# Kernel optimization log

Hardware: AMD Instinct MI355X
Metric: run time of the kernel (lower is better)

The kernel has to match this reference:

```python
import jax, jax.numpy as jnp
import numpy as np

TURBO_BLOCK_SIZE = 64
TURBO_MSE_BITS = 5
QMAX = 2 ** (TURBO_MSE_BITS - 1) - 1  # 15 for symmetric int5
# MSE scale search grid: shrink factors applied to the max-abs scale
SHRINKS = np.linspace(0.4, 1.0, 16)


def mse_quant_dequant(w):
    """Block-wise (block=64, along input dim) symmetric int5 quantize-dequantize.
    Per block, searches a grid of shrunken max-abs scales and keeps the one
    minimizing reconstruction MSE."""
    O, I = w.shape
    wb = w.reshape(O, I // TURBO_BLOCK_SIZE, TURBO_BLOCK_SIZE)
    amax = jnp.max(jnp.abs(wb), axis=-1, keepdims=True)
    base = jnp.maximum(amax, 1e-8) / QMAX
    best_err = jnp.full(amax.shape, jnp.inf, dtype=w.dtype)
    best_scale = base
    for s in SHRINKS:  # fixed small grid, not a data-dim loop
        scale = base * jnp.asarray(s, dtype=w.dtype)
        deq = jnp.clip(jnp.round(wb / scale), -QMAX, QMAX) * scale
        err = jnp.sum((deq - wb) ** 2, axis=-1, keepdims=True)
        upd = err < best_err
        best_err = jnp.where(upd, err, best_err)
        best_scale = jnp.where(upd, scale, best_scale)
    deq = jnp.clip(jnp.round(wb / best_scale), -QMAX, QMAX) * best_scale
    return deq.reshape(O, I)


def turbo_linear(x, w):
    # Straight-through estimator: forward uses quantized weights,
    # gradient flows to w as identity.
    wq = w + jax.lax.stop_gradient(mse_quant_dequant(w) - w)
    return x @ wq.T


def setup_inputs() -> dict:
    key = jax.random.key(0)
    k1, k2, k3 = jax.random.split(key, 3)
    dim, mlp_mult = 2048, 4
    hidden = mlp_mult * dim
    x = jax.random.normal(k1, (4, 2048, dim), dtype=jnp.float32)
    w_fc = jax.random.normal(k2, (hidden, dim), dtype=jnp.float32) * 0.02
    w_proj = jax.random.normal(k3, (dim, hidden), dtype=jnp.float32) * 0.02
    return {"x": x, "w_fc": w_fc, "w_proj": w_proj}


def reference(x, w_fc, w_proj):
    h = jnp.maximum(turbo_linear(x, w_fc), 0.0)  # relu
    return turbo_linear(h * h, w_proj)           # relu-square then proj
```

## Files before the change

### kernel.cpp

```cpp
#include <hip/hip_runtime.h>
#include <hip/hip_bf16.h>

typedef __attribute__((ext_vector_type(8))) __bf16 bf16x8;
typedef __attribute__((ext_vector_type(4))) float f32x4;

__device__ __forceinline__ void gload_lds16(const void* g, void* lds) {
    __builtin_amdgcn_global_load_lds(
        (const __attribute__((address_space(1))) void*)g,
        (__attribute__((address_space(3))) void*)lds, 16, 0, 0);
}

__global__ __launch_bounds__(256) void quant_bf16_kernel(
    const float* __restrict__ w, __hip_bfloat16* __restrict__ wq, int nblk)
{
#pragma clang fp contract(off)
    int b = blockIdx.x * 256 + threadIdx.x;
    if (b >= nblk) return;
    const float4* src = (const float4*)(w + (size_t)b * 64);
    float v[64];
#pragma unroll
    for (int i = 0; i < 16; ++i) {
        float4 t = src[i];
        v[i*4+0] = t.x; v[i*4+1] = t.y; v[i*4+2] = t.z; v[i*4+3] = t.w;
    }
    float amax = 0.0f;
#pragma unroll
    for (int i = 0; i < 64; ++i) amax = fmaxf(amax, fabsf(v[i]));
    float base = fmaxf(amax, 1e-8f) / 15.0f;

    float best_err = __builtin_inff();
    float best_scale = base, best_rs = 0.0f;
    for (int k = 0; k < 16; ++k) {
        double sd = (k == 15) ? 1.0 : ((double)k * (0.6 / 15.0) + 0.4);
        float scale = base * (float)sd;
        float rs = 1.0f / scale;
        float err = 0.0f;
#pragma unroll
        for (int i = 0; i < 64; ++i) {
            float q = rintf(v[i] * rs);
            q = fminf(fmaxf(q, -15.0f), 15.0f);
            float d = q * scale - v[i];
            err = err + d * d;
        }
        if (err < best_err) { best_err = err; best_scale = scale; best_rs = rs; }
    }
    __hip_bfloat16* dst = wq + (size_t)b * 64;
#pragma unroll
    for (int i = 0; i < 64; ++i) {
        float q = rintf(v[i] * best_rs);
        q = fminf(fmaxf(q, -15.0f), 15.0f);
        dst[i] = __float2bfloat16(q * best_scale);
    }
}

__global__ __launch_bounds__(256) void f32_to_bf16_kernel(
    const float* __restrict__ in, __hip_bfloat16* __restrict__ out, int n8)
{
    int i = blockIdx.x * 256 + threadIdx.x;
    if (i >= n8) return;
    const float4* p = (const float4*)(in + (size_t)i * 8);
    float4 a = p[0], b = p[1];
    alignas(16) __hip_bfloat16 r[8];
    r[0] = __float2bfloat16(a.x); r[1] = __float2bfloat16(a.y);
    r[2] = __float2bfloat16(a.z); r[3] = __float2bfloat16(a.w);
    r[4] = __float2bfloat16(b.x); r[5] = __float2bfloat16(b.y);
    r[6] = __float2bfloat16(b.z); r[7] = __float2bfloat16(b.w);
    *(uint4*)(out + (size_t)i * 8) = *(const uint4*)r;
}

#define SB0() __builtin_amdgcn_sched_barrier(0)
#define BARRIER() { SB0(); __builtin_amdgcn_s_barrier(); SB0(); }
#define STAGE(base, eoff, ldsOff) \
    gload_lds16((base) + (size_t)((eoff) + voff), smem + (ldsOff) + wOff)

template <int EPI>
__global__ __launch_bounds__(256, 2) void gemm256_kernel(
    const __hip_bfloat16* __restrict__ A,
    const __hip_bfloat16* __restrict__ B,
    void* __restrict__ Cout, int M, int N, int K)
{
    extern __shared__ char smem[];

    const int t    = threadIdx.x;
    const int lane = t & 63;
    const int w    = t >> 6;
    const int wr   = w >> 1;
    const int wc   = w & 1;
    const int lo   = lane & 15;
    const int hi   = lane >> 4;
    const uint wOff = (uint)w * 1024u;

    const int cpx = gridDim.x >> 3;
    int bid = blockIdx.x;
    bid = (bid & 7) * cpx + (bid >> 3);
    const int nN = N >> 7;
    const int bm = bid / nN;
    const int bn = bid % nN;
    const int rowBase = bm << 8;
    const int colBase = bn << 7;

    const __hip_bfloat16* uA = A + (size_t)rowBase * (size_t)K;
    const __hip_bfloat16* uB = B + (size_t)colBase * (size_t)K;

    const uint voff = ((uint)(t >> 2)) * (uint)K
                    + ((((uint)t & 3u) ^ (((uint)t >> 3) & 3u)) * 8u);
    const uint K64 = (uint)K * 64u;

    const uint laneOff = (uint)lo * 64u
                       + ((((uint)hi) ^ (((uint)lo >> 1) & 3u)) << 4);
    const uint aFB = (uint)wr * 8192u + laneOff;
    const uint bFB = 16384u + (uint)wc * 4096u + laneOff;

    f32x4 acc[8][4] = {};

    STAGE(uA, 0u,     0u);      STAGE(uA, K64,    4096u);
    STAGE(uA, 2u*K64, 8192u);   STAGE(uA, 3u*K64, 12288u);
    STAGE(uB, 0u,     16384u);  STAGE(uB, K64,    20480u);
    asm volatile("s_waitcnt vmcnt(0)" ::: "memory");
    BARRIER();

    const int NT = K >> 5;
    for (int tt = 0; tt < NT; ++tt) {
        const uint bufOff = (uint)(tt & 1) * 24576u;
        const uint nxtOff = bufOff ^ 24576u;
        const bool pf = (tt + 1 < NT);
        const uint kN = ((uint)(tt + 1)) << 5;

        if (pf) {
            STAGE(uA, kN,          nxtOff + 0u);
            STAGE(uA, kN + K64,    nxtOff + 4096u);
            STAGE(uA, kN + 2u*K64, nxtOff + 8192u);
            STAGE(uA, kN + 3u*K64, nxtOff + 12288u);
            STAGE(uB, kN,          nxtOff + 16384u);
            STAGE(uB, kN + K64,    nxtOff + 20480u);
        }
        SB0();

        bf16x8 bfr[4], afr[8];
#pragma unroll
        for (int j = 0; j < 4; ++j)
            bfr[j] = *(const bf16x8*)(smem + bufOff + bFB + (uint)j * 1024u);
#pragma unroll
        for (int i = 0; i < 8; ++i)
            afr[i] = *(const bf16x8*)(smem + bufOff + aFB + (uint)i * 1024u);

        __builtin_amdgcn_s_setprio(1);
#pragma unroll
        for (int i = 0; i < 8; ++i)
#pragma unroll
            for (int j = 0; j < 4; ++j)
                acc[i][j] = __builtin_amdgcn_mfma_f32_16x16x32_bf16(
                    afr[i], bfr[j], acc[i][j], 0, 0, 0);
        __builtin_amdgcn_s_setprio(0);

        if (pf) asm volatile("s_waitcnt vmcnt(0)" ::: "memory");
        BARRIER();
    }

    if (EPI == 0) {
        __hip_bfloat16* Cb = (__hip_bfloat16*)Cout;
#pragma unroll
        for (int i = 0; i < 8; ++i)
#pragma unroll
            for (int j = 0; j < 4; ++j)
#pragma unroll
                for (int r = 0; r < 4; ++r) {
                    size_t row = rowBase + wr*128 + i*16 + hi*4 + r;
                    size_t col = colBase + wc*64 + j*16 + lo;
                    float v = fmaxf(acc[i][j][r], 0.0f);
                    Cb[row * N + col] = __float2bfloat16(v * v);
                }
    } else {
        float* Cf = (float*)Cout;
#pragma unroll
        for (int i = 0; i < 8; ++i)
#pragma unroll
            for (int j = 0; j < 4; ++j)
#pragma unroll
                for (int r = 0; r < 4; ++r) {
                    size_t row = rowBase + wr*128 + i*16 + hi*4 + r;
                    size_t col = colBase + wc*64 + j*16 + lo;
                    Cf[row * N + col] = acc[i][j][r];
                }
    }
}

extern "C" void kernel_launch(void* const* d_in, const int* in_sizes, int n_in,
                              void* d_out, int out_size, void* d_ws, size_t ws_size,
                              hipStream_t stream) {
    const float* x      = (const float*)d_in[0];
    const float* w_fc   = (const float*)d_in[1];
    const float* w_proj = (const float*)d_in[2];
    float* out = (float*)d_out;

    const int DIM = 2048, HID = 8192, M = 8192;

    char* ws = (char*)d_ws;
    __hip_bfloat16* Xb  = (__hip_bfloat16*)ws;
    __hip_bfloat16* Wfc = (__hip_bfloat16*)(ws + (size_t)M * DIM * 2);
    __hip_bfloat16* Wpj = (__hip_bfloat16*)(ws + (size_t)(M * DIM + (size_t)HID * DIM) * 2);
    __hip_bfloat16* H2  = (__hip_bfloat16*)(ws + (size_t)(M * DIM + 2 * (size_t)HID * DIM) * 2);

    (void)hipFuncSetAttribute((const void*)gemm256_kernel<0>,
                              hipFuncAttributeMaxDynamicSharedMemorySize, 49152);
    (void)hipFuncSetAttribute((const void*)gemm256_kernel<1>,
                              hipFuncAttributeMaxDynamicSharedMemorySize, 49152);

    int nblk = HID * DIM / 64;
    quant_bf16_kernel<<<nblk / 256, 256, 0, stream>>>(w_fc, Wfc, nblk);
    quant_bf16_kernel<<<nblk / 256, 256, 0, stream>>>(w_proj, Wpj, nblk);

    int n8 = M * DIM / 8;
    f32_to_bf16_kernel<<<n8 / 256, 256, 0, stream>>>(x, Xb, n8);

    gemm256_kernel<0><<<(M/256)*(HID/128), 256, 49152, stream>>>(
        Xb, Wfc, (void*)H2, M, HID, DIM);

    gemm256_kernel<1><<<(M/256)*(DIM/128), 256, 49152, stream>>>(
        H2, Wpj, (void*)out, M, DIM, HID);
}
```

Measured before the change: 657.3 us.

## Restructure GEMM to 256x256 tiles with 8 waves and interleaved LDS pipeline

Rewrites the GEMM to use 256x256 output tiles with 512 threads (8 waves), 128 KB LDS holding two 64-wide K stages, and an 8-phase schedule. Each phase interleaves global-to-LDS loads of quarter tiles with LDS reads and MFMA quadrants, using fine-grained waitcnt and barriers and a new XOR swizzle. It also merges the two weight quantization launches into one kernel. The aim is more data reuse per tile and better overlap of memory with matrix math, at the cost of occupancy (one block per CU) and tighter sync.

```diff
diff --git a/kernel.cpp b/kernel.cpp
--- a/kernel.cpp
+++ b/kernel.cpp
@@ -10,13 +10,16 @@
         (__attribute__((address_space(3))) void*)lds, 16, 0, 0);
 }
 
-__global__ __launch_bounds__(256) void quant_bf16_kernel(
-    const float* __restrict__ w, __hip_bfloat16* __restrict__ wq, int nblk)
+__global__ __launch_bounds__(256) void quant2_bf16_kernel(
+    const float* __restrict__ w0, __hip_bfloat16* __restrict__ o0,
+    const float* __restrict__ w1, __hip_bfloat16* __restrict__ o1, int nEach)
 {
 #pragma clang fp contract(off)
     int b = blockIdx.x * 256 + threadIdx.x;
-    if (b >= nblk) return;
-    const float4* src = (const float4*)(w + (size_t)b * 64);
+    const float* w; __hip_bfloat16* o; int bb;
+    if (b < nEach) { w = w0; o = o0; bb = b; }
+    else           { w = w1; o = o1; bb = b - nEach; }
+    const float4* src = (const float4*)(w + (size_t)bb * 64);
     float v[64];
 #pragma unroll
     for (int i = 0; i < 16; ++i) {
@@ -44,7 +47,7 @@
         }
         if (err < best_err) { best_err = err; best_scale = scale; best_rs = rs; }
     }
-    __hip_bfloat16* dst = wq + (size_t)b * 64;
+    __hip_bfloat16* dst = o + (size_t)bb * 64;
 #pragma unroll
     for (int i = 0; i < 64; ++i) {
         float q = rintf(v[i] * best_rs);
@@ -70,11 +73,36 @@
 
 #define SB0() __builtin_amdgcn_sched_barrier(0)
 #define BARRIER() { SB0(); __builtin_amdgcn_s_barrier(); SB0(); }
-#define STAGE(base, eoff, ldsOff) \
-    gload_lds16((base) + (size_t)((eoff) + voff), smem + (ldsOff) + wOff)
+#define LGKM0() { asm volatile("s_waitcnt lgkmcnt(0)" ::: "memory"); SB0(); }
+#define LGKM8() { asm volatile("s_waitcnt lgkmcnt(8)" ::: "memory"); SB0(); }
+#define VM8()   { asm volatile("s_waitcnt vmcnt(8)" ::: "memory"); SB0(); }
+#define VM0()   { asm volatile("s_waitcnt vmcnt(0)" ::: "memory"); SB0(); }
+
+#define RD_AQ(aq, bufOff, mq) { \
+  _Pragma("unroll") for (int m_ = 0; m_ < 4; ++m_) { \
+    aq[m_][0] = *(const bf16x8*)(smem + (bufOff) + (mq)*16384u + aRd + (uint)m_*2048u + koff0); \
+    aq[m_][1] = *(const bf16x8*)(smem + (bufOff) + (mq)*16384u + aRd + (uint)m_*2048u + koff1); } }
+
+#define RD_BH(bq, bufOff, nh) { \
+  _Pragma("unroll") for (int n_ = 0; n_ < 2; ++n_) { \
+    bq[n_][0] = *(const bf16x8*)(smem + (bufOff) + 32768u + (nh)*16384u + bRd + (uint)n_*2048u + koff0); \
+    bq[n_][1] = *(const bf16x8*)(smem + (bufOff) + 32768u + (nh)*16384u + bRd + (uint)n_*2048u + koff1); } }
+
+#define MFQ(mq, nh, aq, bq) { \
+  _Pragma("unroll") for (int m_ = 0; m_ < 4; ++m_) \
+  _Pragma("unroll") for (int n_ = 0; n_ < 2; ++n_) { \
+    acc[(mq)*4+m_][(nh)*2+n_] = __builtin_amdgcn_mfma_f32_16x16x32_bf16( \
+        aq[m_][0], bq[n_][0], acc[(mq)*4+m_][(nh)*2+n_],0,0,0); \
+    acc[(mq)*4+m_][(nh)*2+n_] = __builtin_amdgcn_mfma_f32_16x16x32_bf16( \
+        aq[m_][1], bq[n_][1], acc[(mq)*4+m_][(nh)*2+n_],0,0,0); } }
+
+#define STAGE_A(bufbase, r, kk) \
+    gload_lds16(uA + (size_t)(aG[r] + (kk)), smem + (bufbase) + (r)*8192u + wOff)
+#define STAGE_B(bufbase, r, kk) \
+    gload_lds16(uB + (size_t)(bG[r] + (kk)), smem + (bufbase) + 32768u + (r)*8192u + wOff)
 
 template <int EPI>
-__global__ __launch_bounds__(256, 2) void gemm256_kernel(
+__global__ __launch_bounds__(512) void gemm256_kernel(
     const __hip_bfloat16* __restrict__ A,
     const __hip_bfloat16* __restrict__ B,
     void* __restrict__ Cout, int M, int N, int K)
@@ -84,8 +112,8 @@
     const int t    = threadIdx.x;
     const int lane = t & 63;
     const int w    = t >> 6;
-    const int wr   = w >> 1;
-    const int wc   = w & 1;
+    const int wr   = w >> 2;
+    const int wc   = w & 3;
     const int lo   = lane & 15;
     const int hi   = lane >> 4;
     const uint wOff = (uint)w * 1024u;
@@ -93,68 +121,101 @@
     const int cpx = gridDim.x >> 3;
     int bid = blockIdx.x;
     bid = (bid & 7) * cpx + (bid >> 3);
-    const int nN = N >> 7;
+    const int nN = N >> 8;
     const int bm = bid / nN;
     const int bn = bid % nN;
     const int rowBase = bm << 8;
-    const int colBase = bn << 7;
+    const int colBase = bn << 8;
 
     const __hip_bfloat16* uA = A + (size_t)rowBase * (size_t)K;
     const __hip_bfloat16* uB = B + (size_t)colBase * (size_t)K;
 
-    const uint voff = ((uint)(t >> 2)) * (uint)K
-                    + ((((uint)t & 3u) ^ (((uint)t >> 3) & 3u)) * 8u);
-    const uint K64 = (uint)K * 64u;
-
-    const uint laneOff = (uint)lo * 64u
-                       + ((((uint)hi) ^ (((uint)lo >> 1) & 3u)) << 4);
-    const uint aFB = (uint)wr * 8192u + laneOff;
-    const uint bFB = 16384u + (uint)wc * 4096u + laneOff;
+    uint o = wOff + (uint)lane * 16u;
+    uint p = o ^ (((o >> 7) & 7u) << 4);
+    const uint lrow = p >> 7;
+    const uint elem = (p & 127u) >> 1;
+    uint aG[4], bG[4];
+    aG[0] = (0u   + lrow) * (uint)K + elem;
+    aG[1] = (128u + lrow) * (uint)K + elem;
+    aG[2] = (64u  + lrow) * (uint)K + elem;
+    aG[3] = (192u + lrow) * (uint)K + elem;
+    const uint bb = (lrow >> 5) * 64u + (lrow & 31u);
+    bG[0] = (bb +   0u) * (uint)K + elem;
+    bG[1] = (bb + 128u) * (uint)K + elem;
+    bG[2] = (bb +  32u) * (uint)K + elem;
+    bG[3] = (bb + 160u) * (uint)K + elem;
+
+    const uint sw    = (uint)(lo & 7) << 4;
+    const uint aRd   = (uint)wr * 8192u + (uint)lo * 128u;
+    const uint bRd   = (uint)wc * 4096u + (uint)lo * 128u;
+    const uint koff0 = ((uint)hi * 16u)        ^ sw;
+    const uint koff1 = (64u + (uint)hi * 16u)  ^ sw;
 
     f32x4 acc[8][4] = {};
-
-    STAGE(uA, 0u,     0u);      STAGE(uA, K64,    4096u);
-    STAGE(uA, 2u*K64, 8192u);   STAGE(uA, 3u*K64, 12288u);
-    STAGE(uB, 0u,     16384u);  STAGE(uB, K64,    20480u);
-    asm volatile("s_waitcnt vmcnt(0)" ::: "memory");
+    bf16x8 aq[4][2], bq0[2][2], bq1[2][2];
+
+    STAGE_A(0u, 0, 0u); STAGE_A(0u, 1, 0u); STAGE_A(0u, 2, 0u); STAGE_A(0u, 3, 0u);
+    STAGE_B(0u, 0, 0u); STAGE_B(0u, 1, 0u); STAGE_B(0u, 2, 0u); STAGE_B(0u, 3, 0u);
+    STAGE_A(65536u, 0, 64u); STAGE_A(65536u, 1, 64u);
+    STAGE_B(65536u, 0, 64u); STAGE_B(65536u, 1, 64u);
+    asm volatile("s_waitcnt vmcnt(4)" ::: "memory");
     BARRIER();
 
-    const int NT = K >> 5;
-    for (int tt = 0; tt < NT; ++tt) {
-        const uint bufOff = (uint)(tt & 1) * 24576u;
-        const uint nxtOff = bufOff ^ 24576u;
-        const bool pf = (tt + 1 < NT);
-        const uint kN = ((uint)(tt + 1)) << 5;
-
-        if (pf) {
-            STAGE(uA, kN,          nxtOff + 0u);
-            STAGE(uA, kN + K64,    nxtOff + 4096u);
-            STAGE(uA, kN + 2u*K64, nxtOff + 8192u);
-            STAGE(uA, kN + 3u*K64, nxtOff + 12288u);
-            STAGE(uB, kN,          nxtOff + 16384u);
-            STAGE(uB, kN + K64,    nxtOff + 20480u);
-        }
-        SB0();
-
-        bf16x8 bfr[4], afr[8];
-#pragma unroll
-        for (int j = 0; j < 4; ++j)
-            bfr[j] = *(const bf16x8*)(smem + bufOff + bFB + (uint)j * 1024u);
-#pragma unroll
-        for (int i = 0; i < 8; ++i)
-            afr[i] = *(const bf16x8*)(smem + bufOff + aFB + (uint)i * 1024u);
-
-        __builtin_amdgcn_s_setprio(1);
-#pragma unroll
-        for (int i = 0; i < 8; ++i)
-#pragma unroll
-            for (int j = 0; j < 4; ++j)
-                acc[i][j] = __builtin_amdgcn_mfma_f32_16x16x32_bf16(
-                    afr[i], bfr[j], acc[i][j], 0, 0, 0);
-        __builtin_amdgcn_s_setprio(0);
-
-        if (pf) asm volatile("s_waitcnt vmcnt(0)" ::: "memory");
+    const int NI = K >> 7;
+    for (int P = 0; P < NI; ++P) {
+        const bool pf = (P + 1 < NI);
+        const uint kT1 = ((uint)(2 * P + 1)) << 6;
+        const uint kT2 = kT1 + 64u;
+        const uint kT3 = kT1 + 128u;
+
+        RD_AQ(aq, 0u, 0); RD_BH(bq0, 0u, 0);
+        STAGE_B(65536u, 2, kT1); STAGE_B(65536u, 3, kT1);
+        LGKM8();
+        BARRIER(); LGKM0();
+        __builtin_amdgcn_s_setprio(1); MFQ(0, 0, aq, bq0); __builtin_amdgcn_s_setprio(0);
+        VM8(); BARRIER();
+
+        RD_BH(bq1, 0u, 1);
+        STAGE_A(65536u, 2, kT1); STAGE_A(65536u, 3, kT1);
+        BARRIER(); LGKM0();
+        __builtin_amdgcn_s_setprio(1); MFQ(0, 1, aq, bq1); __builtin_amdgcn_s_setprio(0);
+        VM8(); BARRIER();
+
+        RD_AQ(aq, 0u, 1);
+        if (pf) { STAGE_A(0u, 0, kT2); STAGE_A(0u, 1, kT2); }
+        BARRIER(); LGKM0();
+        __builtin_amdgcn_s_setprio(1); MFQ(1, 0, aq, bq0); __builtin_amdgcn_s_setprio(0);
+        VM8(); BARRIER();
+
+        if (pf) { STAGE_B(0u, 0, kT2); STAGE_B(0u, 1, kT2); }
         BARRIER();
+        __builtin_amdgcn_s_setprio(1); MFQ(1, 1, aq, bq1); __builtin_amdgcn_s_setprio(0);
+        if (pf) { VM8(); } else { VM0(); }
+        BARRIER();
+
+        RD_AQ(aq, 65536u, 0); RD_BH(bq0, 65536u, 0);
+        if (pf) { STAGE_B(0u, 2, kT2); STAGE_B(0u, 3, kT2); }
+        LGKM8();
+        BARRIER(); LGKM0();
+        __builtin_amdgcn_s_setprio(1); MFQ(0, 0, aq, bq0); __builtin_amdgcn_s_setprio(0);
+        VM8(); BARRIER();
+
+        RD_BH(bq1, 65536u, 1);
+        if (pf) { STAGE_A(0u, 2, kT2); STAGE_A(0u, 3, kT2); }
+        BARRIER(); LGKM0();
+        __builtin_amdgcn_s_setprio(1); MFQ(0, 1, aq, bq1); __builtin_amdgcn_s_setprio(0);
+        VM8(); BARRIER();
+
+        RD_AQ(aq, 65536u, 1);
+        if (pf) { STAGE_A(65536u, 0, kT3); STAGE_A(65536u, 1, kT3); }
+        BARRIER(); LGKM0();
+        __builtin_amdgcn_s_setprio(1); MFQ(1, 0, aq, bq0); __builtin_amdgcn_s_setprio(0);
+        VM8(); BARRIER();
+
+        if (pf) { STAGE_B(65536u, 0, kT3); STAGE_B(65536u, 1, kT3); }
+        BARRIER();
+        __builtin_amdgcn_s_setprio(1); MFQ(1, 1, aq, bq1); __builtin_amdgcn_s_setprio(0);
+        VM8(); BARRIER();
     }
 
     if (EPI == 0) {
@@ -164,10 +225,10 @@
 #pragma unroll
             for (int j = 0; j < 4; ++j)
 #pragma unroll
-                for (int r = 0; r < 4; ++r) {
-                    size_t row = rowBase + wr*128 + i*16 + hi*4 + r;
-                    size_t col = colBase + wc*64 + j*16 + lo;
-                    float v = fmaxf(acc[i][j][r], 0.0f);
+                for (int rr = 0; rr < 4; ++rr) {
+                    size_t row = rowBase + wr*128 + (i>>2)*64 + (i&3)*16 + hi*4 + rr;
+                    size_t col = colBase + wc*64 + (j>>1)*32 + (j&1)*16 + lo;
+                    float v = fmaxf(acc[i][j][rr], 0.0f);
                     Cb[row * N + col] = __float2bfloat16(v * v);
                 }
     } else {
@@ -177,10 +238,10 @@
 #pragma unroll
             for (int j = 0; j < 4; ++j)
 #pragma unroll
-                for (int r = 0; r < 4; ++r) {
-                    size_t row = rowBase + wr*128 + i*16 + hi*4 + r;
-                    size_t col = colBase + wc*64 + j*16 + lo;
-                    Cf[row * N + col] = acc[i][j][r];
+                for (int rr = 0; rr < 4; ++rr) {
+                    size_t row = rowBase + wr*128 + (i>>2)*64 + (i&3)*16 + hi*4 + rr;
+                    size_t col = colBase + wc*64 + (j>>1)*32 + (j&1)*16 + lo;
+                    Cf[row * N + col] = acc[i][j][rr];
                 }
     }
 }
@@ -202,20 +263,20 @@
     __hip_bfloat16* H2  = (__hip_bfloat16*)(ws + (size_t)(M * DIM + 2 * (size_t)HID * DIM) * 2);
 
     (void)hipFuncSetAttribute((const void*)gemm256_kernel<0>,
-                              hipFuncAttributeMaxDynamicSharedMemorySize, 49152);
+                              hipFuncAttributeMaxDynamicSharedMemorySize, 131072);
     (void)hipFuncSetAttribute((const void*)gemm256_kernel<1>,
-                              hipFuncAttributeMaxDynamicSharedMemorySize, 49152);
+                              hipFuncAttributeMaxDynamicSharedMemorySize, 131072);
 
     int nblk = HID * DIM / 64;
-    quant_bf16_kernel<<<nblk / 256, 256, 0, stream>>>(w_fc, Wfc, nblk);
-    quant_bf16_kernel<<<nblk / 256, 256, 0, stream>>>(w_proj, Wpj, nblk);
+    quant2_bf16_kernel<<<2 * nblk / 256, 256, 0, stream>>>(
+        w_fc, Wfc, w_proj, Wpj, nblk);
 
     int n8 = M * DIM / 8;
     f32_to_bf16_kernel<<<n8 / 256, 256, 0, stream>>>(x, Xb, n8);
 
-    gemm256_kernel<0><<<(M/256)*(HID/128), 256, 49152, stream>>>(
+    gemm256_kernel<0><<<(M/256)*(HID/256), 512, 131072, stream>>>(
         Xb, Wfc, (void*)H2, M, HID, DIM);
 
-    gemm256_kernel<1><<<(M/256)*(DIM/128), 256, 49152, stream>>>(
+    gemm256_kernel<1><<<(M/256)*(DIM/256), 512, 131072, stream>>>(
         H2, Wpj, (void*)out, M, DIM, HID);
 }
```

Result: faster. 628.5 us (-4.4%).
